# Kernel tuning notes

Hardware: AMD Instinct MI355X
Metric: run time of the kernel (lower is better)

Reference implementation:

```python
import jax, jax.numpy as jnp
import numpy as np

B, T, F, H = 128, 1024, 64, 256


def _lstm_cell(x, h, c, W_ih, W_hh, b):
    # x: [B,F], h,c: [B,H]; gate order i,f,g,o (PyTorch convention)
    gates = x @ W_ih.T + h @ W_hh.T + b  # [B,4H]
    i, f, g, o = jnp.split(gates, 4, axis=-1)
    i, f, o = jax.nn.sigmoid(i), jax.nn.sigmoid(f), jax.nn.sigmoid(o)
    g = jnp.tanh(g)
    c = f * c + i * g
    h = o * jnp.tanh(c)
    return h, c


def setup_inputs() -> dict:
    key = jax.random.key(0)
    ks = jax.random.split(key, 10)
    s = 1.0 / np.sqrt(H)
    inp = {
        "ts_batch": jax.random.normal(ks[0], (B, T, F), jnp.float32),
        "W_ih_enc": jax.random.uniform(ks[1], (4 * H, F), jnp.float32, -s, s),
        "W_hh_enc": jax.random.uniform(ks[2], (4 * H, H), jnp.float32, -s, s),
        "b_enc": jax.random.uniform(ks[3], (4 * H,), jnp.float32, -s, s),
        "W_ih_dec": jax.random.uniform(ks[4], (4 * H, F), jnp.float32, -s, s),
        "W_hh_dec": jax.random.uniform(ks[5], (4 * H, H), jnp.float32, -s, s),
        "b_dec": jax.random.uniform(ks[6], (4 * H,), jnp.float32, -s, s),
        "W_out": jax.random.uniform(ks[7], (F, H), jnp.float32, -s, s),
        "b_out": jax.random.uniform(ks[8], (F,), jnp.float32, -s, s),
    }
    return inp


def reference(ts_batch, W_ih_enc, W_hh_enc, b_enc, W_ih_dec, W_hh_dec, b_dec, W_out, b_out):
    batch = ts_batch.shape[0]
    hidden = W_hh_enc.shape[1]
    xs = jnp.swapaxes(ts_batch, 0, 1)  # [T,B,F]

    # ---- encoder: full-sequence LSTM, keep only final (h,c) ----
    def enc_step(carry, x):
        h, c = carry
        h, c = _lstm_cell(x, h, c, W_ih_enc, W_hh_enc, b_enc)
        return (h, c), None

    h0 = jnp.zeros((batch, hidden), ts_batch.dtype)
    (h, c), _ = jax.lax.scan(enc_step, (h0, h0), xs)

    # ---- decoder: iterate timesteps in reverse; emit projection of the
    # hidden state BEFORE consuming the input at that step (training branch) ----
    def dec_step(carry, x):
        h, c = carry
        out = h @ W_out.T + b_out  # [B,F]
        h, c = _lstm_cell(x, h, c, W_ih_dec, W_hh_dec, b_dec)
        return (h, c), out

    _, outs_rev = jax.lax.scan(dec_step, (h, c), xs[::-1])  # [T,B,F], reversed time
    return jnp.swapaxes(outs_rev[::-1], 0, 1)  # [B,T,F]
```

## Files before the change

### kernel.cpp

```cpp
#include <hip/hip_runtime.h>
#include <hip/hip_bf16.h>


#define Bb 128
#define Tt 1024
#define Ff 64
#define Hh 256

typedef _Float16 h16;
typedef __attribute__((ext_vector_type(8))) _Float16 h16x8;
typedef __attribute__((ext_vector_type(4))) float f32x4;

#define WENC_OFF 0
#define WDEC_OFF 327680
#define WOUT_OFF 655360
#define HBUF_OFF 671744
#define FLAGS_BYTE_OFF 1474560

__device__ __forceinline__ float fast_sigmoid(float x) {
  float e = __expf(-fabsf(x));
  float s = __builtin_amdgcn_rcpf(1.f + e);
  return x >= 0.f ? s : 1.f - s;
}
__device__ __forceinline__ float fast_tanh(float x) {
  float e = __expf(-2.f * fabsf(x));
  float r = (1.f - e) * __builtin_amdgcn_rcpf(1.f + e);
  return x >= 0.f ? r : -r;
}

__global__ void lstm_prep(const float* __restrict__ Wih_e, const float* __restrict__ Whh_e,
                          const float* __restrict__ Wih_d, const float* __restrict__ Whh_d,
                          const float* __restrict__ Wout, h16* __restrict__ ws16,
                          unsigned int* __restrict__ flags) {
  int e = blockIdx.x * 256 + threadIdx.x;
  if (e < 16) flags[e] = 0u;
  if (e < 655360) {
    int r = e;
    const float* Wih = Wih_e; const float* Whh = Whh_e;
    int off = WENC_OFF;
    if (r >= 327680) { r -= 327680; Wih = Wih_d; Whh = Whh_d; off = WDEC_OFF; }
    int j    = r & 7;
    int lane = (r >> 3) & 63;
    int kt   = (r >> 9) % 10;
    int tmp  = (r >> 9) / 10;
    int nt   = tmp & 7;
    int w    = (tmp >> 3) & 3;
    int q    = tmp >> 5;
    int g = nt >> 1, ct = nt & 1;
    int col = q * 128 + w * 32 + ct * 16 + (lane & 15);
    int row = g * 256 + col;
    int k = kt * 32 + (lane >> 4) * 8 + j;
    float v = (k < 64) ? Wih[row * 64 + k] : Whh[row * 256 + (k - 64)];
    ws16[off + r] = (h16)v;
  } else if (e < 655360 + 16384) {
    int r = e - 655360;
    int j    = r & 7;
    int lane = (r >> 3) & 63;
    int kt   = (r >> 9) & 7;
    int wt   = (r >> 12) & 1;
    int q    = (r >> 13) & 1;
    int f = q * 32 + wt * 16 + (lane & 15);
    int k = kt * 32 + (lane >> 4) * 8 + j;
    ws16[WOUT_OFF + r] = (h16)Wout[f * 256 + k];
  }
}

__global__ __launch_bounds__(256, 1) void lstm_main(
    const float* __restrict__ ts,
    const float* __restrict__ b_enc, const float* __restrict__ b_dec,
    const float* __restrict__ b_out,
    const h16* __restrict__ wsW, h16* __restrict__ hbuf,
    unsigned int* flags, float* __restrict__ out) {
  const int tid = threadIdx.x;
  const int wg = blockIdx.x;
  const int grp = wg & 7, q = wg >> 3;
  const int w = tid >> 6, lane = tid & 63;
  const int n16 = lane & 15, quad = lane >> 4;
  const int b0 = grp * 16;
  const int partner = wg ^ 8;

  __shared__ h16 xh[2][16][328];
  __shared__ h16x8 woutLds[1024];

  h16x8 wf[8][10];
  {
    const h16x8* wsrc = (const h16x8*)(wsW + WENC_OFF);
#pragma unroll
    for (int nt = 0; nt < 8; ++nt)
#pragma unroll
      for (int kt = 0; kt < 10; ++kt)
        wf[nt][kt] = wsrc[(((q * 4 + w) * 8 + nt) * 10 + kt) * 64 + lane];
  }
  float bias8[8];
#pragma unroll
  for (int nt = 0; nt < 8; ++nt) {
    int g = nt >> 1, ct = nt & 1;
    bias8[nt] = b_enc[g * 256 + q * 128 + w * 32 + ct * 16 + n16];
  }
  const float bo = b_out[q * 32 + w * 16 + n16];

  float c8[8];
#pragma unroll
  for (int i = 0; i < 8; ++i) c8[i] = 0.f;

  for (int i = tid; i < 16 * 264; i += 256) {
    int m = i / 264;
    xh[0][m][64 + (i - m * 264)] = (h16)0.f;
  }
  const int m_x = tid >> 4, ks_x = (tid & 15) * 4;
  {
    const f32x4 xv0 = *(const f32x4*)(ts + ((size_t)(b0 + m_x) * Tt + 0) * Ff + ks_x);
#pragma unroll
    for (int u = 0; u < 4; ++u) xh[0][m_x][ks_x + u] = (h16)xv0[u];
  }
  __syncthreads();

  for (int t = 0; t < 2048; ++t) {
    const int nb = t & 1, nxt = nb ^ 1;
    const bool dec = (t >= 1024);

    if (t > 0) {
      while (__hip_atomic_load(&flags[partner], __ATOMIC_ACQUIRE,
                               __HIP_MEMORY_SCOPE_AGENT) < (unsigned int)t)
        __builtin_amdgcn_s_sleep(1);
    }

    if (t == 1024) {
      const h16x8* wsrc2 = (const h16x8*)(wsW + WDEC_OFF);
#pragma unroll
      for (int nt = 0; nt < 8; ++nt)
#pragma unroll
        for (int kt = 0; kt < 10; ++kt)
          wf[nt][kt] = wsrc2[(((q * 4 + w) * 8 + nt) * 10 + kt) * 64 + lane];
#pragma unroll
      for (int nt = 0; nt < 8; ++nt) {
        int g = nt >> 1, ct = nt & 1;
        bias8[nt] = b_dec[g * 256 + q * 128 + w * 32 + ct * 16 + n16];
      }
      const h16x8* wo = (const h16x8*)(wsW + WOUT_OFF) + q * 1024;
      for (int i = tid; i < 1024; i += 256) woutLds[i] = wo[i];
      __syncthreads();
    }

    h16x8 a[10];
    const h16* xrow = &xh[nb][n16][0];
#pragma unroll
    for (int kt = 0; kt < 2; ++kt)
      a[kt] = *(const h16x8*)(xrow + kt * 32 + quad * 8);
    if (q == 0) {
#pragma unroll
      for (int i = 0; i < 4; ++i)
        a[2 + i] = *(const h16x8*)(xrow + (2 + i) * 32 + quad * 8);
    } else {
#pragma unroll
      for (int i = 0; i < 4; ++i)
        a[6 + i] = *(const h16x8*)(xrow + (6 + i) * 32 + quad * 8);
    }
    if (t > 0) {
      const h16x8* ps = (const h16x8*)(hbuf + ((size_t)partner * 2 + ((t + 1) & 1)) * 2048);
      if (q == 0) {
#pragma unroll
        for (int i = 0; i < 4; ++i) a[6 + i] = ps[n16 * 16 + i * 4 + quad];
      } else {
#pragma unroll
        for (int i = 0; i < 4; ++i) a[2 + i] = ps[n16 * 16 + i * 4 + quad];
      }
    } else {
      h16x8 z;
#pragma unroll
      for (int i = 0; i < 8; ++i) z[i] = (h16)0.f;
      if (q == 0) { a[6] = z; a[7] = z; a[8] = z; a[9] = z; }
      else        { a[2] = z; a[3] = z; a[4] = z; a[5] = z; }
    }

    f32x4 xv;
#pragma unroll
    for (int u = 0; u < 4; ++u) xv[u] = 0.f;
    if (t + 1 < 2048) {
      int xi = (t + 1 < 1024) ? (t + 1) : (2047 - (t + 1));
      xv = *(const f32x4*)(ts + ((size_t)(b0 + m_x) * Tt + xi) * Ff + ks_x);
    }

    f32x4 acc[8];
#pragma unroll
    for (int nt = 0; nt < 8; ++nt) {
      f32x4 v; v[0] = bias8[nt]; v[1] = bias8[nt]; v[2] = bias8[nt]; v[3] = bias8[nt];
      acc[nt] = v;
    }
#pragma unroll
    for (int kt = 0; kt < 10; ++kt)
#pragma unroll
      for (int nt = 0; nt < 8; ++nt)
        acc[nt] = __builtin_amdgcn_mfma_f32_16x16x32_f16(a[kt], wf[nt][kt], acc[nt], 0, 0, 0);

    h16 hv[8];
#pragma unroll
    for (int ct = 0; ct < 2; ++ct)
#pragma unroll
      for (int r = 0; r < 4; ++r) {
        float i_ = fast_sigmoid(acc[0 + ct][r]);
        float f_ = fast_sigmoid(acc[2 + ct][r]);
        float g_ = fast_tanh(acc[4 + ct][r]);
        float o_ = fast_sigmoid(acc[6 + ct][r]);
        float cv = f_ * c8[ct * 4 + r] + i_ * g_;
        c8[ct * 4 + r] = cv;
        hv[ct * 4 + r] = (h16)(o_ * fast_tanh(cv));
      }

    if (dec && w < 2) {
      f32x4 ao; ao[0] = bo; ao[1] = bo; ao[2] = bo; ao[3] = bo;
#pragma unroll
      for (int kt = 0; kt < 8; ++kt)
        ao = __builtin_amdgcn_mfma_f32_16x16x32_f16(a[2 + kt], woutLds[(w * 8 + kt) * 64 + lane], ao, 0, 0, 0);
      int tpos = 2047 - t;
      int f = q * 32 + w * 16 + n16;
#pragma unroll
      for (int r = 0; r < 4; ++r) {
        int m = quad * 4 + r;
        out[((size_t)(b0 + m) * Tt + tpos) * Ff + f] = ao[r];
      }
    }

    {
      h16* hb = hbuf + ((size_t)wg * 2 + (t & 1)) * 2048;
#pragma unroll
      for (int ct = 0; ct < 2; ++ct)
#pragma unroll
        for (int r = 0; r < 4; ++r) {
          int m = quad * 4 + r;
          int colLocal = w * 32 + ct * 16 + n16;
          xh[nxt][m][64 + q * 128 + colLocal] = hv[ct * 4 + r];
          hb[m * 128 + colLocal] = hv[ct * 4 + r];
        }
      if (t + 1 < 2048) {
#pragma unroll
        for (int u = 0; u < 4; ++u) xh[nxt][m_x][ks_x + u] = (h16)xv[u];
      }
    }

    __threadfence();
    __syncthreads();
    if (t < 2047 && tid == 0)
      __hip_atomic_store(&flags[wg], (unsigned int)(t + 1), __ATOMIC_RELEASE,
                         __HIP_MEMORY_SCOPE_AGENT);
  }
}

extern "C" void kernel_launch(void* const* d_in, const int* in_sizes, int n_in,
                              void* d_out, int out_size, void* d_ws, size_t ws_size,
                              hipStream_t stream) {
  const float* ts  = (const float*)d_in[0];
  const float* Wie = (const float*)d_in[1];
  const float* Whe = (const float*)d_in[2];
  const float* be  = (const float*)d_in[3];
  const float* Wid = (const float*)d_in[4];
  const float* Whd = (const float*)d_in[5];
  const float* bd  = (const float*)d_in[6];
  const float* Wo  = (const float*)d_in[7];
  const float* bo  = (const float*)d_in[8];

  h16* ws16 = (h16*)d_ws;
  unsigned int* flags = (unsigned int*)((char*)d_ws + FLAGS_BYTE_OFF);
  float* out = (float*)d_out;

  lstm_prep<<<2624, 256, 0, stream>>>(Wie, Whe, Wid, Whd, Wo, ws16, flags);
  lstm_main<<<16, 256, 0, stream>>>(ts, be, bd, bo, ws16, ws16 + HBUF_OFF, flags, out);
}
```

Baseline: 10.56 ms.

## Overlap partner wait with local MFMAs and use per-wave relaxed flag signalling

Moves the cross-workgroup spin-wait after the MFMAs over the input and the workgroup's own hidden half, so only the partner half waits on the flag. Hidden-state exchange now goes through LDS, then coalesced 64-bit relaxed atomic stores. Each wave bumps the flag with a fetch_add after draining its own stores, replacing the threadfence, barrier and single release store. The sigmoid and tanh are also simplified to exp2 plus rcp forms. The relaxed ordering with no acquire or release fences risks memory-ordering hazards, and the new activation forms may overflow or lose precision for large inputs.

```diff
diff --git a/kernel.cpp b/kernel.cpp
--- a/kernel.cpp
+++ b/kernel.cpp
@@ -10,6 +10,7 @@
 typedef _Float16 h16;
 typedef __attribute__((ext_vector_type(8))) _Float16 h16x8;
 typedef __attribute__((ext_vector_type(4))) float f32x4;
+typedef __attribute__((ext_vector_type(2))) unsigned long long u64x2;
 
 #define WENC_OFF 0
 #define WDEC_OFF 327680
@@ -17,15 +18,11 @@
 #define HBUF_OFF 671744
 #define FLAGS_BYTE_OFF 1474560
 
-__device__ __forceinline__ float fast_sigmoid(float x) {
-  float e = __expf(-fabsf(x));
-  float s = __builtin_amdgcn_rcpf(1.f + e);
-  return x >= 0.f ? s : 1.f - s;
-}
-__device__ __forceinline__ float fast_tanh(float x) {
-  float e = __expf(-2.f * fabsf(x));
-  float r = (1.f - e) * __builtin_amdgcn_rcpf(1.f + e);
-  return x >= 0.f ? r : -r;
+__device__ __forceinline__ float sigm(float x) {
+  return __builtin_amdgcn_rcpf(1.f + __builtin_amdgcn_exp2f(-1.442695041f * x));
+}
+__device__ __forceinline__ float tanh_f(float x) {
+  return 2.f * __builtin_amdgcn_rcpf(1.f + __builtin_amdgcn_exp2f(-2.885390082f * x)) - 1.f;
 }
 
 __global__ void lstm_prep(const float* __restrict__ Wih_e, const float* __restrict__ Whh_e,
@@ -119,12 +116,6 @@
     const int nb = t & 1, nxt = nb ^ 1;
     const bool dec = (t >= 1024);
 
-    if (t > 0) {
-      while (__hip_atomic_load(&flags[partner], __ATOMIC_ACQUIRE,
-                               __HIP_MEMORY_SCOPE_AGENT) < (unsigned int)t)
-        __builtin_amdgcn_s_sleep(1);
-    }
-
     if (t == 1024) {
       const h16x8* wsrc2 = (const h16x8*)(wsW + WDEC_OFF);
 #pragma unroll
@@ -147,31 +138,11 @@
 #pragma unroll
     for (int kt = 0; kt < 2; ++kt)
       a[kt] = *(const h16x8*)(xrow + kt * 32 + quad * 8);
-    if (q == 0) {
-#pragma unroll
-      for (int i = 0; i < 4; ++i)
-        a[2 + i] = *(const h16x8*)(xrow + (2 + i) * 32 + quad * 8);
-    } else {
-#pragma unroll
-      for (int i = 0; i < 4; ++i)
-        a[6 + i] = *(const h16x8*)(xrow + (6 + i) * 32 + quad * 8);
-    }
-    if (t > 0) {
-      const h16x8* ps = (const h16x8*)(hbuf + ((size_t)partner * 2 + ((t + 1) & 1)) * 2048);
-      if (q == 0) {
-#pragma unroll
-        for (int i = 0; i < 4; ++i) a[6 + i] = ps[n16 * 16 + i * 4 + quad];
-      } else {
-#pragma unroll
-        for (int i = 0; i < 4; ++i) a[2 + i] = ps[n16 * 16 + i * 4 + quad];
-      }
-    } else {
-      h16x8 z;
-#pragma unroll
-      for (int i = 0; i < 8; ++i) z[i] = (h16)0.f;
-      if (q == 0) { a[6] = z; a[7] = z; a[8] = z; a[9] = z; }
-      else        { a[2] = z; a[3] = z; a[4] = z; a[5] = z; }
-    }
+    const int ownBase = (q == 0) ? 2 : 6;
+    const int parBase = (q == 0) ? 6 : 2;
+#pragma unroll
+    for (int i = 0; i < 4; ++i)
+      a[ownBase + i] = *(const h16x8*)(xrow + (ownBase + i) * 32 + quad * 8);
 
     f32x4 xv;
 #pragma unroll
@@ -188,24 +159,97 @@
       acc[nt] = v;
     }
 #pragma unroll
-    for (int kt = 0; kt < 10; ++kt)
+    for (int kt = 0; kt < 2; ++kt)
 #pragma unroll
       for (int nt = 0; nt < 8; ++nt)
         acc[nt] = __builtin_amdgcn_mfma_f32_16x16x32_f16(a[kt], wf[nt][kt], acc[nt], 0, 0, 0);
+#pragma unroll
+    for (int i = 0; i < 4; ++i)
+#pragma unroll
+      for (int nt = 0; nt < 8; ++nt)
+        acc[nt] = __builtin_amdgcn_mfma_f32_16x16x32_f16(a[ownBase + i], wf[nt][ownBase + i], acc[nt], 0, 0, 0);
+
+    if (t > 0) {
+      unsigned int want = 4u * (unsigned int)t;
+      while (__hip_atomic_load(&flags[partner], __ATOMIC_RELAXED,
+                               __HIP_MEMORY_SCOPE_AGENT) < want) {}
+      asm volatile("" ::: "memory");
+      const unsigned long long* ps64 =
+          (const unsigned long long*)(hbuf + ((size_t)partner * 2 + ((t + 1) & 1)) * 2048);
+      const int gb = n16 * 32 + quad * 2;
+      unsigned long long gld[8];
+#pragma unroll
+      for (int i = 0; i < 4; ++i) {
+        gld[2 * i + 0] = __hip_atomic_load(&ps64[gb + i * 8 + 0], __ATOMIC_RELAXED,
+                                           __HIP_MEMORY_SCOPE_AGENT);
+        gld[2 * i + 1] = __hip_atomic_load(&ps64[gb + i * 8 + 1], __ATOMIC_RELAXED,
+                                           __HIP_MEMORY_SCOPE_AGENT);
+      }
+#pragma unroll
+      for (int i = 0; i < 4; ++i) {
+        union { unsigned long long u[2]; h16x8 v; } cv;
+        cv.u[0] = gld[2 * i + 0];
+        cv.u[1] = gld[2 * i + 1];
+        a[parBase + i] = cv.v;
+      }
+    } else {
+      h16x8 z;
+#pragma unroll
+      for (int i = 0; i < 8; ++i) z[i] = (h16)0.f;
+#pragma unroll
+      for (int i = 0; i < 4; ++i) a[parBase + i] = z;
+    }
+
+#pragma unroll
+    for (int i = 0; i < 4; ++i)
+#pragma unroll
+      for (int nt = 0; nt < 8; ++nt)
+        acc[nt] = __builtin_amdgcn_mfma_f32_16x16x32_f16(a[parBase + i], wf[nt][parBase + i], acc[nt], 0, 0, 0);
 
     h16 hv[8];
 #pragma unroll
     for (int ct = 0; ct < 2; ++ct)
 #pragma unroll
       for (int r = 0; r < 4; ++r) {
-        float i_ = fast_sigmoid(acc[0 + ct][r]);
-        float f_ = fast_sigmoid(acc[2 + ct][r]);
-        float g_ = fast_tanh(acc[4 + ct][r]);
-        float o_ = fast_sigmoid(acc[6 + ct][r]);
+        float i_ = sigm(acc[0 + ct][r]);
+        float f_ = sigm(acc[2 + ct][r]);
+        float g_ = tanh_f(acc[4 + ct][r]);
+        float o_ = sigm(acc[6 + ct][r]);
         float cv = f_ * c8[ct * 4 + r] + i_ * g_;
         c8[ct * 4 + r] = cv;
-        hv[ct * 4 + r] = (h16)(o_ * fast_tanh(cv));
-      }
+        hv[ct * 4 + r] = (h16)(o_ * tanh_f(cv));
+      }
+
+#pragma unroll
+    for (int ct = 0; ct < 2; ++ct)
+#pragma unroll
+      for (int r = 0; r < 4; ++r) {
+        int m = quad * 4 + r;
+        xh[nxt][m][64 + q * 128 + w * 32 + ct * 16 + n16] = hv[ct * 4 + r];
+      }
+    if (t + 1 < 2048) {
+#pragma unroll
+      for (int u = 0; u < 4; ++u) xh[nxt][m_x][ks_x + u] = (h16)xv[u];
+    }
+
+    __syncthreads();
+
+    {
+      const int rm = tid >> 4, rp = tid & 15;
+      u64x2 hval = *(const u64x2*)&xh[nxt][rm][64 + q * 128 + rp * 8];
+      unsigned long long* hb64 =
+          (unsigned long long*)(hbuf + ((size_t)wg * 2 + (t & 1)) * 2048);
+      __hip_atomic_store(&hb64[tid * 2 + 0], hval[0], __ATOMIC_RELAXED,
+                         __HIP_MEMORY_SCOPE_AGENT);
+      __hip_atomic_store(&hb64[tid * 2 + 1], hval[1], __ATOMIC_RELAXED,
+                         __HIP_MEMORY_SCOPE_AGENT);
+    }
+
+    asm volatile("s_waitcnt vmcnt(0)" ::: "memory");
+    if (t < 2047 && (tid & 63) == 0)
+      __hip_atomic_fetch_add(&flags[wg], 1u, __ATOMIC_RELAXED,
+                             __HIP_MEMORY_SCOPE_AGENT);
+    asm volatile("" ::: "memory");
 
     if (dec && w < 2) {
       f32x4 ao; ao[0] = bo; ao[1] = bo; ao[2] = bo; ao[3] = bo;
@@ -220,29 +264,6 @@
         out[((size_t)(b0 + m) * Tt + tpos) * Ff + f] = ao[r];
       }
     }
-
-    {
-      h16* hb = hbuf + ((size_t)wg * 2 + (t & 1)) * 2048;
-#pragma unroll
-      for (int ct = 0; ct < 2; ++ct)
-#pragma unroll
-        for (int r = 0; r < 4; ++r) {
-          int m = quad * 4 + r;
-          int colLocal = w * 32 + ct * 16 + n16;
-          xh[nxt][m][64 + q * 128 + colLocal] = hv[ct * 4 + r];
-          hb[m * 128 + colLocal] = hv[ct * 4 + r];
-        }
-      if (t + 1 < 2048) {
-#pragma unroll
-        for (int u = 0; u < 4; ++u) xh[nxt][m_x][ks_x + u] = (h16)xv[u];
-      }
-    }
-
-    __threadfence();
-    __syncthreads();
-    if (t < 2047 && tid == 0)
-      __hip_atomic_store(&flags[wg], (unsigned int)(t + 1), __ATOMIC_RELEASE,
-                         __HIP_MEMORY_SCOPE_AGENT);
   }
 }
 
```

After: 20.55 ms. 94.6% more time.
